# Kernel tuning notes

Hardware: AMD Instinct MI355X
Metric: run time of the kernel (lower is better)

The kernel has to match this reference:

```python
import jax, jax.numpy as jnp
import numpy as np

B, N, DIM = 2, 2048, 1024
HEADS, DIM_HEAD = 8, 64
INNER = HEADS * DIM_HEAD  # 512
EPS = 1e-5  # fp32 branch of the source LayerNorm


def setup_inputs() -> dict:
    key = jax.random.key(0)
    ks = jax.random.split(key, 5)
    x = jax.random.normal(ks[0], (B, N, DIM), dtype=jnp.float32)
    g = jnp.ones((DIM,), dtype=jnp.float32)  # LayerNorm gain init
    # Linear weights stored as (in, out) so y = x @ W. Source zero-inits
    # to_out; we use small random values so the baseline output is nonzero.
    wq = jax.random.normal(ks[1], (DIM, INNER), dtype=jnp.float32) * 0.02
    wkv = jax.random.normal(ks[2], (DIM, 2 * INNER), dtype=jnp.float32) * 0.02
    wo = jax.random.normal(ks[3], (INNER, DIM), dtype=jnp.float32) * 0.02
    return {"x": x, "g": g, "wq": wq, "wkv": wkv, "wo": wo}


def reference(x, g, wq, wkv, wo):
    # Custom LayerNorm from the source: statistics over dim=1 (sequence axis!)
    mean = jnp.mean(x, axis=1, keepdims=True)
    var = jnp.var(x, axis=1, keepdims=True)  # unbiased=False
    xn = (x - mean) * jax.lax.rsqrt(var + EPS) * g  # g broadcasts on last dim

    q = xn @ wq                      # [b, n, inner]
    kv = xn @ wkv                    # [b, n, 2*inner]
    k, v = jnp.split(kv, 2, axis=-1)

    def split_heads(t):  # b n (h d) -> b h n d
        b, n, _ = t.shape
        return t.reshape(b, n, HEADS, DIM_HEAD).transpose(0, 2, 1, 3)

    q, k, v = map(split_heads, (q, k, v))
    q = q * (DIM_HEAD ** -0.5)

    sim = jnp.einsum('bhid,bhjd->bhij', q, k)   # [b, h, n, n]
    attn = jax.nn.softmax(sim, axis=-1)
    out = jnp.einsum('bhij,bhjd->bhid', attn, v)  # [b, h, n, d]

    out = out.transpose(0, 2, 1, 3).reshape(B, N, INNER)  # b h n d -> b n (h d)
    return out @ wo  # [b, n, dim]
```

## Files before the change

### kernel.cpp

```cpp
#include <hip/hip_runtime.h>
#include <hip/hip_bf16.h>
#include <stdint.h>


#define B_ 2
#define N_ 2048
#define DIM_ 1024
#define DH_ 64
#define INNER_ 512
#define ROWS_ 4096
#define POSTRIDE 2097152
#define BHSTRIDE 131072

#define QSCALE 0.18033688011112042f

typedef __bf16 bf16x8 __attribute__((ext_vector_type(8)));
typedef float floatx4 __attribute__((ext_vector_type(4)));

#if __has_builtin(__builtin_amdgcn_exp2f)
#define EXP2(x) __builtin_amdgcn_exp2f(x)
#else
#define EXP2(x) exp2f(x)
#endif

__device__ __forceinline__ ushort f2bf(float f) {
    union { float f; uint32_t u; } v; v.f = f;
    uint32_t u = v.u;
    u += 0x7fffu + ((u >> 16) & 1u);
    return (ushort)(u >> 16);
}
__device__ __forceinline__ uint32_t pkbf(float a, float b) {
    return (uint32_t)f2bf(a) | ((uint32_t)f2bf(b) << 16);
}
__device__ __forceinline__ size_t frag_off(int m, int k, int nkc) {
    return ((size_t)((m >> 4) * nkc + (k >> 5)) * 64 +
            (size_t)((m & 15) | (((k >> 3) & 3) << 4))) * 8 + (k & 7);
}

__global__ __launch_bounds__(256) void setup_fused(
    const float* __restrict__ x, float* __restrict__ ps, float* __restrict__ pq,
    const float* __restrict__ wq, const float* __restrict__ wkv,
    const float* __restrict__ wo, ushort* __restrict__ wqkv_f,
    ushort* __restrict__ wo_f) {
    __shared__ float tile[32][33];
    int bid = blockIdx.x;
    if (bid < 256) {
        int gd = (bid & 7) * 256 + threadIdx.x;
        int ch = bid >> 3;
        int b = gd >> 10;
        const float* p = x + (size_t)(b * N_ + ch * 64) * DIM_ + (gd & 1023);
        float s = 0.f, q = 0.f;
#pragma unroll 4
        for (int n = 0; n < 64; ++n) { float v = p[(size_t)n * DIM_]; s += v; q += v * v; }
        ps[ch * 2048 + gd] = s;
        pq[ch * 2048 + gd] = q;
        return;
    }
    int t = bid - 256;
    const float* src; ushort* dst; int C, K, k0, ncol0, nglob0; float scale;
    if (t < 512) {
        int kt = t >> 4, nt = t & 15;
        src = wq; dst = wqkv_f; C = 512; K = 1024; scale = QSCALE;
        k0 = kt * 32; ncol0 = nt * 32; nglob0 = ncol0;
    } else if (t < 1536) {
        int u = t - 512; int kt = u >> 5, nt = u & 31;
        src = wkv; dst = wqkv_f; C = 1024; K = 1024; scale = 1.f;
        k0 = kt * 32; ncol0 = nt * 32; nglob0 = 512 + ncol0;
    } else {
        int u = t - 1536; int kt = u >> 5, nt = u & 31;
        src = wo; dst = wo_f; C = 1024; K = 512; scale = 1.f;
        k0 = kt * 32; ncol0 = nt * 32; nglob0 = ncol0;
    }
    int ti = threadIdx.x >> 5, tj = threadIdx.x & 31;
#pragma unroll
    for (int p = 0; p < 4; ++p)
        tile[ti + 8 * p][tj] = src[(size_t)(k0 + ti + 8 * p) * C + ncol0 + tj] * scale;
    __syncthreads();
    if (threadIdx.x < 128) {
        int nl = threadIdx.x & 31, kc8 = threadIdx.x >> 5;
        union { ushort us[8]; uint4 v; } u;
#pragma unroll
        for (int ii = 0; ii < 8; ++ii) u.us[ii] = f2bf(tile[kc8 * 8 + ii][nl]);
        *(uint4*)&dst[frag_off(nglob0 + nl, k0 + kc8 * 8, K >> 5)] = u.v;
    }
}

__global__ __launch_bounds__(256) void finalize_norm(
    const float* __restrict__ ps, const float* __restrict__ pq,
    const float* __restrict__ x, const float* __restrict__ g,
    ushort* __restrict__ xnf) {
    __shared__ float s4[4][64], q4[4][64], aa[64], bb[64];
    int t = threadIdx.x;
    int b = blockIdx.x >> 8, slab = (blockIdx.x >> 4) & 15, nch = blockIdx.x & 15;
    int c0 = slab * 64;
    {
        int c = t & 63, grp = t >> 6;
        float s = 0.f, q = 0.f;
#pragma unroll
        for (int ch = 0; ch < 8; ++ch) {
            int o = (grp * 8 + ch) * 2048 + b * 1024 + c0 + c;
            s += ps[o]; q += pq[o];
        }
        s4[grp][c] = s; q4[grp][c] = q;
    }
    __syncthreads();
    if (t < 64) {
        float s = s4[0][t] + s4[1][t] + s4[2][t] + s4[3][t];
        float q = q4[0][t] + q4[1][t] + q4[2][t] + q4[3][t];
        float mean = s * (1.f / N_);
        float var = q * (1.f / N_) - mean * mean;
        float rstd = rsqrtf(var + 1e-5f);
        float a = rstd * g[c0 + t];
        aa[t] = a; bb[t] = -mean * a;
    }
    __syncthreads();
    int c4 = (t & 15) * 4, ro = t >> 4;
#pragma unroll
    for (int it = 0; it < 8; ++it) {
        int r = nch * 128 + it * 16 + ro;
        int m = b * 2048 + r;
        float4 xv = *(const float4*)&x[(size_t)m * DIM_ + c0 + c4];
        float v0 = xv.x * aa[c4 + 0] + bb[c4 + 0];
        float v1 = xv.y * aa[c4 + 1] + bb[c4 + 1];
        float v2 = xv.z * aa[c4 + 2] + bb[c4 + 2];
        float v3 = xv.w * aa[c4 + 3] + bb[c4 + 3];
        uint2 u; u.x = pkbf(v0, v1); u.y = pkbf(v2, v3);
        *(uint2*)&xnf[frag_off(m, c0 + c4, 32)] = u;
    }
}

template <int NKC>
__device__ __forceinline__ void gemm_core(
    const ushort* __restrict__ pA, const ushort* __restrict__ pB,
    floatx4 (&acc)[4][4]) {
    constexpr int TS = NKC * 512;
    bf16x8 a0[4], b0[4], a1[4], b1[4];
#pragma unroll
    for (int i = 0; i < 4; ++i) {
        a0[i] = *(const bf16x8*)(pA + (size_t)i * TS);
        b0[i] = *(const bf16x8*)(pB + (size_t)i * TS);
    }
    for (int kc = 0; kc < NKC; kc += 2) {
#pragma unroll
        for (int i = 0; i < 4; ++i) {
            a1[i] = *(const bf16x8*)(pA + (size_t)i * TS + (size_t)(kc + 1) * 512);
            b1[i] = *(const bf16x8*)(pB + (size_t)i * TS + (size_t)(kc + 1) * 512);
        }
#pragma unroll
        for (int mi = 0; mi < 4; ++mi)
#pragma unroll
            for (int ni = 0; ni < 4; ++ni)
                acc[mi][ni] = __builtin_amdgcn_mfma_f32_16x16x32_bf16(
                    a0[mi], b0[ni], acc[mi][ni], 0, 0, 0);
        if (kc + 2 < NKC) {
#pragma unroll
            for (int i = 0; i < 4; ++i) {
                a0[i] = *(const bf16x8*)(pA + (size_t)i * TS + (size_t)(kc + 2) * 512);
                b0[i] = *(const bf16x8*)(pB + (size_t)i * TS + (size_t)(kc + 2) * 512);
            }
        }
#pragma unroll
        for (int mi = 0; mi < 4; ++mi)
#pragma unroll
            for (int ni = 0; ni < 4; ++ni)
                acc[mi][ni] = __builtin_amdgcn_mfma_f32_16x16x32_bf16(
                    a1[mi], b1[ni], acc[mi][ni], 0, 0, 0);
    }
}

__global__ __launch_bounds__(128) void gemm_qkv(
    const ushort* __restrict__ xnf, const ushort* __restrict__ wf,
    ushort* __restrict__ qf, ushort* __restrict__ kf, ushort* __restrict__ vf) {
    int tx = threadIdx.x, w = tx >> 6, l = tx & 63;
    int lr = l & 15, lq = l >> 4;
    int bx = blockIdx.x, by = blockIdx.y;
    const ushort* pA = xnf + (size_t)(bx * 4) * 32 * 512 + l * 8;
    const ushort* pB = wf + (size_t)(by * 8 + w * 4) * 32 * 512 + l * 8;
    floatx4 acc[4][4] = {};
    gemm_core<32>(pA, pB, acc);
    int col0 = by * 128 + w * 64;
    int bb2 = (bx * 64) >> 11;
    if (by < 8) {
        ushort* qkbase = (by < 4) ? qf : kf;
#pragma unroll
        for (int ni = 0; ni < 4; ++ni) {
            int col = col0 + 16 * ni + lr;
            int hh = (col >> 6) & 7, d = col & 63;
            ushort* base = qkbase + (size_t)(bb2 * 8 + hh) * BHSTRIDE
                           + (d >> 5) * 512 + ((d >> 3) & 3) * 128 + (d & 7)
                           + (4 * lq) * 8;
#pragma unroll
            for (int mi = 0; mi < 4; ++mi) {
                size_t o2 = (size_t)((bx * 4 + mi) & 127) * 1024;
#pragma unroll
                for (int reg = 0; reg < 4; ++reg)
                    base[o2 + reg * 8] = f2bf(acc[mi][ni][reg]);
            }
        }
    } else {
#pragma unroll
        for (int ni = 0; ni < 4; ++ni) {
            int cv = col0 - 1024 + 16 * ni + lr;
            int hh = cv >> 6, d = cv & 63;
            ushort* base = vf + (size_t)(bb2 * 8 + hh) * BHSTRIDE
                           + (d >> 4) * 32768 + (d & 15) * 8;
#pragma unroll
            for (int mi = 0; mi < 4; ++mi) {
                int nn = (bx * 64 + 16 * mi + 4 * lq) & 2047;
                uint2 u;
                u.x = pkbf(acc[mi][ni][0], acc[mi][ni][1]);
                u.y = pkbf(acc[mi][ni][2], acc[mi][ni][3]);
                *(uint2*)&base[(nn >> 5) * 512 + ((nn >> 3) & 3) * 128 + (nn & 7)] = u;
            }
        }
    }
}

__global__ __launch_bounds__(128) void gemm_out(
    const ushort* __restrict__ af, const ushort* __restrict__ wf,
    float* __restrict__ out) {
    int tx = threadIdx.x, w = tx >> 6, l = tx & 63;
    int lr = l & 15, lq = l >> 4;
    int bx = blockIdx.x, by = blockIdx.y;
    const ushort* pA = af + (size_t)(bx * 4) * 16 * 512 + l * 8;
    const ushort* pB = wf + (size_t)(by * 8 + w * 4) * 16 * 512 + l * 8;
    floatx4 acc[4][4] = {};
    gemm_core<16>(pA, pB, acc);
    int col0 = by * 128 + w * 64;
#pragma unroll
    for (int mi = 0; mi < 4; ++mi)
#pragma unroll
        for (int ni = 0; ni < 4; ++ni) {
            int col = col0 + 16 * ni + lr;
#pragma unroll
            for (int reg = 0; reg < 4; ++reg) {
                int row = bx * 64 + 16 * mi + 4 * lq + reg;
                out[(size_t)row * 1024 + col] = acc[mi][ni][reg];
            }
        }
}

__global__ __launch_bounds__(256, 2) void flash_attn(
    const ushort* __restrict__ qf, const ushort* __restrict__ kf,
    const ushort* __restrict__ vf, float* __restrict__ po,
    float* __restrict__ pl, int nkt) {
    __shared__ __align__(16) ushort sP[4][32 * 72];

    const int tx = threadIdx.x;
    const int w = tx >> 6, l = tx & 63;
    const int lr = l & 15, lq = l >> 4;
    const int qt = blockIdx.x, bh = blockIdx.y, sp = blockIdx.z;
    const int qbase = qt * 128;
    const int kbase = sp * nkt * 64;

    const ushort* qfb = qf + (size_t)bh * BHSTRIDE + (size_t)(qbase + 32 * w) * 64 + l * 8;
    const ushort* kfb = kf + (size_t)bh * BHSTRIDE + (size_t)kbase * 64 + l * 8;
    const ushort* vfb = vf + (size_t)bh * BHSTRIDE + (size_t)kbase * 16 + l * 8;
    ushort* sPw = &sP[w][0];

    bf16x8 bq[2][2];
#pragma unroll
    for (int qq = 0; qq < 2; ++qq)
#pragma unroll
        for (int s = 0; s < 2; ++s)
            bq[qq][s] = *(const bf16x8*)(qfb + qq * 1024 + s * 512);

    floatx4 o[2][4] = {};
    float lsum[2] = {0.f, 0.f};

    bf16x8 ak[2][8], bv[2][8];
    auto load_kv = [&](int kt, int buf) {
        const ushort* kp = kfb + (size_t)kt * 4096;
        const ushort* vp = vfb + (size_t)kt * 1024;
#pragma unroll
        for (int kk = 0; kk < 4; ++kk) {
            ak[buf][kk * 2 + 0] = *(const bf16x8*)(kp + kk * 1024);
            ak[buf][kk * 2 + 1] = *(const bf16x8*)(kp + kk * 1024 + 512);
        }
#pragma unroll
        for (int dt = 0; dt < 4; ++dt) {
            bv[buf][dt * 2 + 0] = *(const bf16x8*)(vp + dt * 32768);
            bv[buf][dt * 2 + 1] = *(const bf16x8*)(vp + dt * 32768 + 512);
        }
    };
    auto compute = [&](int buf) {
        floatx4 c[4][2] = {};
#pragma unroll
        for (int s = 0; s < 2; ++s)
#pragma unroll
            for (int kk = 0; kk < 4; ++kk)
#pragma unroll
                for (int qq = 0; qq < 2; ++qq)
                    c[kk][qq] = __builtin_amdgcn_mfma_f32_16x16x32_bf16(
                        ak[buf][kk * 2 + s], bq[qq][s], c[kk][qq], 0, 0, 0);
#pragma unroll
        for (int kk = 0; kk < 4; ++kk)
#pragma unroll
            for (int qq = 0; qq < 2; ++qq) {
                float e0 = EXP2(c[kk][qq][0]);
                float e1 = EXP2(c[kk][qq][1]);
                float e2 = EXP2(c[kk][qq][2]);
                float e3 = EXP2(c[kk][qq][3]);
                lsum[qq] += (e0 + e1) + (e2 + e3);
                uint2 u; u.x = pkbf(e0, e1); u.y = pkbf(e2, e3);
                *(uint2*)&sPw[(16 * qq + lr) * 72 + 16 * kk + 4 * lq] = u;
            }
#pragma unroll
        for (int s = 0; s < 2; ++s) {
            bf16x8 ap[2];
#pragma unroll
            for (int mi = 0; mi < 2; ++mi)
                ap[mi] = *(const bf16x8*)&sPw[(16 * mi + lr) * 72 + 32 * s + 8 * lq];
#pragma unroll
            for (int mi = 0; mi < 2; ++mi)
#pragma unroll
                for (int dt = 0; dt < 4; ++dt)
                    o[mi][dt] = __builtin_amdgcn_mfma_f32_16x16x32_bf16(
                        ap[mi], bv[buf][dt * 2 + s], o[mi][dt], 0, 0, 0);
        }
    };

    load_kv(0, 0);
    int kt = 0;
    for (; kt + 2 <= nkt; kt += 2) {
        load_kv(kt + 1, 1);
        compute(0);
        if (kt + 2 < nkt) load_kv(kt + 2, 0);
        compute(1);
    }
    if (kt < nkt) compute(0);

#pragma unroll
    for (int qq = 0; qq < 2; ++qq) {
        lsum[qq] += __shfl_xor(lsum[qq], 16);
        lsum[qq] += __shfl_xor(lsum[qq], 32);
    }
    float* pob = po + (size_t)sp * POSTRIDE;
    if (lq == 0) {
#pragma unroll
        for (int qq = 0; qq < 2; ++qq)
            pl[((size_t)sp * 16 + bh) * N_ + qbase + 32 * w + 16 * qq + lr] = lsum[qq];
    }
    const size_t obase = (size_t)bh * N_;
#pragma unroll
    for (int mi = 0; mi < 2; ++mi)
#pragma unroll
        for (int dt = 0; dt < 4; ++dt)
#pragma unroll
            for (int reg = 0; reg < 4; ++reg) {
                int row = qbase + 32 * w + 16 * mi + 4 * lq + reg;
                pob[(obase + row) * DH_ + 16 * dt + lr] = o[mi][dt][reg];
            }
}

__global__ __launch_bounds__(256) void merge_attn(
    const float* __restrict__ po, const float* __restrict__ pl,
    ushort* __restrict__ attnf, int nsplit) {
    int idx = blockIdx.x * 256 + threadIdx.x;
    int d4 = (idx & 15) * 4;
    int h = (idx >> 4) & 7;
    int rowg = idx >> 7;
    int b = rowg >> 11, r = rowg & 2047;
    size_t pbase = ((size_t)b * 8 + h) * N_ + r;
    float4 acc = *(const float4*)&po[pbase * DH_ + d4];
    float lv = pl[pbase];
    for (int s = 1; s < nsplit; ++s) {
        float4 a1 = *(const float4*)&po[(size_t)s * POSTRIDE + pbase * DH_ + d4];
        acc.x += a1.x; acc.y += a1.y; acc.z += a1.z; acc.w += a1.w;
        lv += pl[((size_t)s * 16) * N_ + pbase];
    }
    float inv = 1.f / lv;
    uint2 u;
    u.x = pkbf(acc.x * inv, acc.y * inv);
    u.y = pkbf(acc.z * inv, acc.w * inv);
    *(uint2*)&attnf[frag_off(rowg, h * DH_ + d4, 16)] = u;
}

extern "C" void kernel_launch(void* const* d_in, const int* in_sizes, int n_in,
                              void* d_out, int out_size, void* d_ws, size_t ws_size,
                              hipStream_t stream) {
    const float* x   = (const float*)d_in[0];
    const float* g   = (const float*)d_in[1];
    const float* wq  = (const float*)d_in[2];
    const float* wkv = (const float*)d_in[3];
    const float* wo  = (const float*)d_in[4];
    float* out = (float*)d_out;

    char* ws = (char*)d_ws;
    float*  psum   = (float*)(ws + 0);
    float*  psqr   = (float*)(ws + 262144);
    ushort* xnf    = (ushort*)(ws + 524288);
    ushort* wqkv_f = (ushort*)(ws + 8912896);
    ushort* wo_f   = (ushort*)(ws + 12058624);
    ushort* qfb    = (ushort*)(ws + 13107200);
    ushort* kfb    = (ushort*)(ws + 17301504);
    ushort* vfb    = (ushort*)(ws + 21495808);
    ushort* attnf  = (ushort*)(ws + 25690112);
    float*  plb    = (float*)(ws + 29884416);
    float*  pob    = (float*)(ws + 30408704);

    const int nsplit = (ws_size >= (size_t)66 * 1024 * 1024) ? 4
                     : (ws_size >= (size_t)48 * 1024 * 1024) ? 2 : 1;

    setup_fused<<<2304, 256, 0, stream>>>(x, psum, psqr, wq, wkv, wo, wqkv_f, wo_f);
    finalize_norm<<<512, 256, 0, stream>>>(psum, psqr, x, g, xnf);
    gemm_qkv<<<dim3(64, 12), 128, 0, stream>>>(xnf, wqkv_f, qfb, kfb, vfb);
    flash_attn<<<dim3(16, 16, nsplit), 256, 0, stream>>>(qfb, kfb, vfb, pob, plb, 32 / nsplit);
    merge_attn<<<2048, 256, 0, stream>>>(pob, plb, attnf, nsplit);
    gemm_out<<<dim3(64, 8), 128, 0, stream>>>(attnf, wo_f, out);
}
```

Baseline: 162.4 us.

## Double query rows per wave in flash attention and single-buffer K/V prefetch

Each wave now handles 64 query rows instead of 32, so each block covers 256 queries and the grid is halved in x. Every K/V tile loaded from global memory is therefore reused across twice as many queries. The explicit K/V double buffer is replaced by one buffer: the next K tile is prefetched after the QK MFMAs and V is loaded at the top of each iteration. This lowers K/V traffic and frees registers for the larger accumulators, but it halves the number of blocks and exposes more V load latency.

Measured after the change: 163.2 us. No clear change (+0.5%).

```diff
diff --git a/kernel.cpp b/kernel.cpp
--- a/kernel.cpp
+++ b/kernel.cpp
@@ -244,59 +244,66 @@
     const ushort* __restrict__ qf, const ushort* __restrict__ kf,
     const ushort* __restrict__ vf, float* __restrict__ po,
     float* __restrict__ pl, int nkt) {
-    __shared__ __align__(16) ushort sP[4][32 * 72];
+    __shared__ __align__(16) ushort sP[4][64 * 72];
 
     const int tx = threadIdx.x;
     const int w = tx >> 6, l = tx & 63;
     const int lr = l & 15, lq = l >> 4;
     const int qt = blockIdx.x, bh = blockIdx.y, sp = blockIdx.z;
-    const int qbase = qt * 128;
-    const int kbase = sp * nkt * 64;
-
-    const ushort* qfb = qf + (size_t)bh * BHSTRIDE + (size_t)(qbase + 32 * w) * 64 + l * 8;
-    const ushort* kfb = kf + (size_t)bh * BHSTRIDE + (size_t)kbase * 64 + l * 8;
-    const ushort* vfb = vf + (size_t)bh * BHSTRIDE + (size_t)kbase * 16 + l * 8;
+    const int qbase = qt * 256 + w * 64;
+
+    const ushort* qfb = qf + (size_t)bh * BHSTRIDE + (size_t)(qt * 16 + w * 4) * 1024 + l * 8;
+    const ushort* kfb = kf + (size_t)bh * BHSTRIDE + (size_t)(sp * nkt * 4) * 1024 + l * 8;
+    const ushort* vfb = vf + (size_t)bh * BHSTRIDE + (size_t)(sp * nkt * 2) * 512 + l * 8;
     ushort* sPw = &sP[w][0];
 
-    bf16x8 bq[2][2];
-#pragma unroll
-    for (int qq = 0; qq < 2; ++qq)
+    bf16x8 bq[4][2];
+#pragma unroll
+    for (int qq = 0; qq < 4; ++qq)
 #pragma unroll
         for (int s = 0; s < 2; ++s)
             bq[qq][s] = *(const bf16x8*)(qfb + qq * 1024 + s * 512);
 
-    floatx4 o[2][4] = {};
-    float lsum[2] = {0.f, 0.f};
-
-    bf16x8 ak[2][8], bv[2][8];
-    auto load_kv = [&](int kt, int buf) {
-        const ushort* kp = kfb + (size_t)kt * 4096;
-        const ushort* vp = vfb + (size_t)kt * 1024;
-#pragma unroll
-        for (int kk = 0; kk < 4; ++kk) {
-            ak[buf][kk * 2 + 0] = *(const bf16x8*)(kp + kk * 1024);
-            ak[buf][kk * 2 + 1] = *(const bf16x8*)(kp + kk * 1024 + 512);
-        }
+    floatx4 o[4][4] = {};
+    float lsum[4] = {0.f, 0.f, 0.f, 0.f};
+
+    bf16x8 ak[8], bv[8];
+#pragma unroll
+    for (int kk = 0; kk < 4; ++kk) {
+        ak[kk * 2 + 0] = *(const bf16x8*)(kfb + kk * 1024);
+        ak[kk * 2 + 1] = *(const bf16x8*)(kfb + kk * 1024 + 512);
+    }
+
+    for (int kt = 0; kt < nkt; ++kt) {
 #pragma unroll
         for (int dt = 0; dt < 4; ++dt) {
-            bv[buf][dt * 2 + 0] = *(const bf16x8*)(vp + dt * 32768);
-            bv[buf][dt * 2 + 1] = *(const bf16x8*)(vp + dt * 32768 + 512);
-        }
-    };
-    auto compute = [&](int buf) {
-        floatx4 c[4][2] = {};
+            bv[dt * 2 + 0] = *(const bf16x8*)(vfb + dt * 32768 + (kt * 2 + 0) * 512);
+            bv[dt * 2 + 1] = *(const bf16x8*)(vfb + dt * 32768 + (kt * 2 + 1) * 512);
+        }
+
+        floatx4 c[4][4] = {};
 #pragma unroll
         for (int s = 0; s < 2; ++s)
 #pragma unroll
             for (int kk = 0; kk < 4; ++kk)
 #pragma unroll
-                for (int qq = 0; qq < 2; ++qq)
+                for (int qq = 0; qq < 4; ++qq)
                     c[kk][qq] = __builtin_amdgcn_mfma_f32_16x16x32_bf16(
-                        ak[buf][kk * 2 + s], bq[qq][s], c[kk][qq], 0, 0, 0);
+                        ak[kk * 2 + s], bq[qq][s], c[kk][qq], 0, 0, 0);
+
+        if (kt + 1 < nkt) {
+            const ushort* kp = kfb + (size_t)(kt + 1) * 4096;
+#pragma unroll
+            for (int kk = 0; kk < 4; ++kk) {
+                ak[kk * 2 + 0] = *(const bf16x8*)(kp + kk * 1024);
+                ak[kk * 2 + 1] = *(const bf16x8*)(kp + kk * 1024 + 512);
+            }
+        }
+
 #pragma unroll
         for (int kk = 0; kk < 4; ++kk)
 #pragma unroll
-            for (int qq = 0; qq < 2; ++qq) {
+            for (int qq = 0; qq < 4; ++qq) {
                 float e0 = EXP2(c[kk][qq][0]);
                 float e1 = EXP2(c[kk][qq][1]);
                 float e2 = EXP2(c[kk][qq][2]);
@@ -305,50 +312,41 @@
                 uint2 u; u.x = pkbf(e0, e1); u.y = pkbf(e2, e3);
                 *(uint2*)&sPw[(16 * qq + lr) * 72 + 16 * kk + 4 * lq] = u;
             }
+
 #pragma unroll
         for (int s = 0; s < 2; ++s) {
-            bf16x8 ap[2];
-#pragma unroll
-            for (int mi = 0; mi < 2; ++mi)
+            bf16x8 ap[4];
+#pragma unroll
+            for (int mi = 0; mi < 4; ++mi)
                 ap[mi] = *(const bf16x8*)&sPw[(16 * mi + lr) * 72 + 32 * s + 8 * lq];
 #pragma unroll
-            for (int mi = 0; mi < 2; ++mi)
+            for (int mi = 0; mi < 4; ++mi)
 #pragma unroll
                 for (int dt = 0; dt < 4; ++dt)
                     o[mi][dt] = __builtin_amdgcn_mfma_f32_16x16x32_bf16(
-                        ap[mi], bv[buf][dt * 2 + s], o[mi][dt], 0, 0, 0);
-        }
-    };
-
-    load_kv(0, 0);
-    int kt = 0;
-    for (; kt + 2 <= nkt; kt += 2) {
-        load_kv(kt + 1, 1);
-        compute(0);
-        if (kt + 2 < nkt) load_kv(kt + 2, 0);
-        compute(1);
-    }
-    if (kt < nkt) compute(0);
-
-#pragma unroll
-    for (int qq = 0; qq < 2; ++qq) {
+                        ap[mi], bv[dt * 2 + s], o[mi][dt], 0, 0, 0);
+        }
+    }
+
+#pragma unroll
+    for (int qq = 0; qq < 4; ++qq) {
         lsum[qq] += __shfl_xor(lsum[qq], 16);
         lsum[qq] += __shfl_xor(lsum[qq], 32);
     }
     float* pob = po + (size_t)sp * POSTRIDE;
     if (lq == 0) {
 #pragma unroll
-        for (int qq = 0; qq < 2; ++qq)
-            pl[((size_t)sp * 16 + bh) * N_ + qbase + 32 * w + 16 * qq + lr] = lsum[qq];
+        for (int qq = 0; qq < 4; ++qq)
+            pl[((size_t)sp * 16 + bh) * N_ + qbase + 16 * qq + lr] = lsum[qq];
     }
     const size_t obase = (size_t)bh * N_;
 #pragma unroll
-    for (int mi = 0; mi < 2; ++mi)
+    for (int mi = 0; mi < 4; ++mi)
 #pragma unroll
         for (int dt = 0; dt < 4; ++dt)
 #pragma unroll
             for (int reg = 0; reg < 4; ++reg) {
-                int row = qbase + 32 * w + 16 * mi + 4 * lq + reg;
+                int row = qbase + 16 * mi + 4 * lq + reg;
                 pob[(obase + row) * DH_ + 16 * dt + lr] = o[mi][dt][reg];
             }
 }
@@ -405,7 +403,7 @@
     setup_fused<<<2304, 256, 0, stream>>>(x, psum, psqr, wq, wkv, wo, wqkv_f, wo_f);
     finalize_norm<<<512, 256, 0, stream>>>(psum, psqr, x, g, xnf);
     gemm_qkv<<<dim3(64, 12), 128, 0, stream>>>(xnf, wqkv_f, qfb, kfb, vfb);
-    flash_attn<<<dim3(16, 16, nsplit), 256, 0, stream>>>(qfb, kfb, vfb, pob, plb, 32 / nsplit);
+    flash_attn<<<dim3(8, 16, nsplit), 256, 0, stream>>>(qfb, kfb, vfb, pob, plb, 32 / nsplit);
     merge_attn<<<2048, 256, 0, stream>>>(pob, plb, attnf, nsplit);
     gemm_out<<<dim3(64, 8), 128, 0, stream>>>(attnf, wo_f, out);
 }
```
